# Performance work log

Hardware: AMD Instinct MI355X
Metric: run time of the kernel (lower is better)

## Reference

```python
import jax, jax.numpy as jnp
import numpy as np

N, E, DIM, EDIM = 40000, 640000, 128, 128
EPS = 1e-5

def _layer_norm(x, gamma, beta):
    mu = jnp.mean(x, axis=-1, keepdims=True)
    var = jnp.mean(jnp.square(x - mu), axis=-1, keepdims=True)
    return (x - mu) * jax.lax.rsqrt(var + EPS) * gamma + beta

def setup_inputs() -> dict:
    key = jax.random.key(0)
    ks = jax.random.split(key, 24)
    def lin(k, din, dout):
        k1, k2 = jax.random.split(k)
        lim = 1.0 / np.sqrt(din)
        return (jax.random.uniform(k1, (din, dout), jnp.float32, -lim, lim),
                jax.random.uniform(k2, (dout,), jnp.float32, -lim, lim))
    w_src, b_src = lin(ks[0], DIM, DIM)
    w_dst, b_dst = lin(ks[1], DIM, DIM)
    w_eg,  b_eg  = lin(ks[2], EDIM, DIM)
    w_msg, b_msg = lin(ks[3], DIM, DIM)
    w_n1,  b_n1  = lin(ks[4], 2 * DIM, DIM)
    w_n2,  b_n2  = lin(ks[5], DIM, DIM)
    w_e1,  b_e1  = lin(ks[6], EDIM + 2 * DIM, EDIM)
    w_e2,  b_e2  = lin(ks[7], EDIM, EDIM)
    return {
        'h': jax.random.normal(ks[8], (N, DIM), jnp.float32),
        'e': jax.random.normal(ks[9], (E, EDIM), jnp.float32),
        'src': jax.random.randint(ks[10], (E,), 0, N, jnp.int32),
        'dst': jax.random.randint(ks[11], (E,), 0, N, jnp.int32),
        'w_src': w_src, 'b_src': b_src, 'w_dst': w_dst, 'b_dst': b_dst,
        'w_eg': w_eg, 'b_eg': b_eg, 'w_msg': w_msg, 'b_msg': b_msg,
        'w_n1': w_n1, 'b_n1': b_n1, 'w_n2': w_n2, 'b_n2': b_n2,
        'w_e1': w_e1, 'b_e1': b_e1, 'w_e2': w_e2, 'b_e2': b_e2,
        'g_n': jnp.ones((DIM,), jnp.float32), 'bt_n': jnp.zeros((DIM,), jnp.float32),
        'g_e': jnp.ones((EDIM,), jnp.float32), 'bt_e': jnp.zeros((EDIM,), jnp.float32),
    }

def reference(h, e, src, dst, w_src, b_src, w_dst, b_dst, w_eg, b_eg,
              w_msg, b_msg, w_n1, b_n1, w_n2, b_n2, w_e1, b_e1, w_e2, b_e2,
              g_n, bt_n, g_e, bt_e):
    # Project on nodes once, then gather per edge (same math as projecting gathered feats)
    h_src_proj = h @ w_src + b_src          # [N, DIM]
    h_dst_proj = h @ w_dst + b_dst          # [N, DIM]
    msg_all = h @ w_msg + b_msg             # [N, DIM]
    gate_logits = h_src_proj[src] + h_dst_proj[dst] + (e @ w_eg + b_eg)  # [E, DIM]
    src_msg = msg_all[src]                  # [E, DIM]
    m = jax.nn.sigmoid(gate_logits) * src_msg
    agg = jax.ops.segment_sum(m, dst, num_segments=N)  # [N, DIM]
    nu = jnp.concatenate([h, agg], axis=-1) @ w_n1 + b_n1
    nu = jax.nn.silu(nu) @ w_n2 + b_n2
    h_new = _layer_norm(h + nu, g_n, bt_n)
    e_input = jnp.concatenate([e, src_msg, msg_all[dst]], axis=-1)  # [E, EDIM+2*DIM]
    eu = jax.nn.silu(e_input @ w_e1 + b_e1) @ w_e2 + b_e2
    e_new = _layer_norm(e + eu, g_e, bt_e)
    return h_new, e_new
```

## Files before the change

### kernel.cpp

```cpp
#include <hip/hip_runtime.h>
#include <hip/hip_bf16.h>
#include <stdint.h>

typedef __hip_bfloat16 bf16;
typedef __attribute__((ext_vector_type(8))) short short8;
typedef __attribute__((ext_vector_type(4))) float f32x4;
typedef __attribute__((ext_vector_type(4))) float f4v;

#define DIMN 128
#define BM 64
#define EPSLN 1e-5f

__device__ __forceinline__ float sigm(float x) { return 1.0f / (1.0f + __expf(-x)); }

__device__ __forceinline__ float bfb2f(unsigned short u) {
    union { uint32_t i; float f; } v; v.i = ((uint32_t)u) << 16; return v.f;
}
__device__ __forceinline__ unsigned short f2bfb(float f) {
    union { float f; uint32_t i; } v; v.f = f;
    uint32_t x = v.i;
    return (unsigned short)((x + 0x7FFFu + ((x >> 16) & 1u)) >> 16);
}

template<int F32>
__device__ __forceinline__ float ld(const void* p, size_t i) {
    if (F32) return ((const float*)p)[i];
    else     return bfb2f(((const unsigned short*)p)[i]);
}
template<int F32>
__device__ __forceinline__ void st(void* p, size_t i, float v) {
    if (F32) ((float*)p)[i] = v;
    else     ((unsigned short*)p)[i] = f2bfb(v);
}
template<int F32>
__device__ __forceinline__ void st_nt(void* p, size_t i, float v) {
    if (F32) __builtin_nontemporal_store(v, (float*)p + i);
    else     __builtin_nontemporal_store(f2bfb(v), (unsigned short*)p + i);
}
template<int F32>
__device__ __forceinline__ void load8(const void* p, size_t elem, float v[8]) {
    if (F32) {
        const f4v* q = (const f4v*)((const float*)p + elem);
        f4v a = q[0], b = q[1];
        v[0]=a.x; v[1]=a.y; v[2]=a.z; v[3]=a.w;
        v[4]=b.x; v[5]=b.y; v[6]=b.z; v[7]=b.w;
    } else {
        short8 s = *(const short8*)((const short*)p + elem);
#pragma unroll
        for (int j = 0; j < 8; ++j) v[j] = bfb2f((unsigned short)s[j]);
    }
}
template<int F32>
__device__ __forceinline__ void load8_nt(const void* p, size_t elem, float v[8]) {
    if (F32) {
        const f4v* q = (const f4v*)((const float*)p + elem);
        f4v a = __builtin_nontemporal_load(q);
        f4v b = __builtin_nontemporal_load(q + 1);
        v[0]=a.x; v[1]=a.y; v[2]=a.z; v[3]=a.w;
        v[4]=b.x; v[5]=b.y; v[6]=b.z; v[7]=b.w;
    } else {
        short8 s = __builtin_nontemporal_load((const short8*)((const short*)p + elem));
#pragma unroll
        for (int j = 0; j < 8; ++j) v[j] = bfb2f((unsigned short)s[j]);
    }
}

__device__ __forceinline__ uint32_t xaddr(int r, int k) {
    return (uint32_t)(r * 768 + ((k * 2) ^ ((r & 7) << 4)));
}
__device__ __forceinline__ uint32_t uaddr(int r, int k) {
    return (uint32_t)(r * 768 + 512 + ((k * 2) ^ ((r & 7) << 4)));
}
__device__ __forceinline__ uint32_t haddr(int r, int k) {
    return (uint32_t)(r * 256 + ((k * 2) ^ ((r & 7) << 4)));
}
__device__ __forceinline__ uint32_t x2addr(int r, int k) {
    return (uint32_t)(r * 512 + ((k * 2) ^ ((r & 7) << 4)));
}

__device__ __forceinline__ void atomic_pk_add_bf16(unsigned short* addr, uint32_t data2) {
    unsigned long long a = (unsigned long long)addr;
    asm volatile("global_atomic_pk_add_bf16 %0, %1, off" : : "v"(a), "v"(data2) : "memory");
}

__global__ void detect_dtype_kernel(const uint32_t* __restrict__ w, int* __restrict__ flag) {
    if (threadIdx.x == 0 && blockIdx.x == 0) {
        int c = 0;
        for (int i = 0; i < 64; ++i) {
            uint32_t lo = w[i] & 0xFFFFu;
            int e = (int)((lo >> 7) & 0xFF);
            if (e >= 90 && e <= 140) ++c;
        }
        *flag = (c < 32) ? 1 : 0;
    }
}

template<int F32>
__device__ void prep_body(
    const void* w_eg, const void* w_e1, const void* w_e2,
    const void* w_src, const void* w_dst, const void* w_msg,
    const void* w_n1, const void* w_n2,
    unsigned short* wtg, unsigned short* wt1, unsigned short* wt2,
    unsigned short* wts, unsigned short* wtd, unsigned short* wtm,
    unsigned short* wn1t, unsigned short* wn2t)
{
    int idx = blockIdx.x * 256 + threadIdx.x;
    if (idx < 16384) {
        int c = idx >> 7, k = idx & 127;
        wtg[idx] = f2bfb(ld<F32>(w_eg, (size_t)k * 128 + c));
    } else if (idx < 32768) {
        int i = idx - 16384; int c = i >> 7, k = i & 127;
        wt2[i] = f2bfb(ld<F32>(w_e2, (size_t)k * 128 + c));
    } else if (idx < 81920) {
        int i = idx - 32768; int c = i / 384, k = i % 384;
        wt1[i] = f2bfb(ld<F32>(w_e1, (size_t)k * 128 + c));
    } else if (idx < 98304) {
        int i = idx - 81920; int c = i >> 7, k = i & 127;
        wts[i] = f2bfb(ld<F32>(w_src, (size_t)k * 128 + c));
    } else if (idx < 114688) {
        int i = idx - 98304; int c = i >> 7, k = i & 127;
        wtd[i] = f2bfb(ld<F32>(w_dst, (size_t)k * 128 + c));
    } else if (idx < 131072) {
        int i = idx - 114688; int c = i >> 7, k = i & 127;
        wtm[i] = f2bfb(ld<F32>(w_msg, (size_t)k * 128 + c));
    } else if (idx < 163840) {
        int i = idx - 131072; int c = i >> 8, k = i & 255;
        wn1t[i] = f2bfb(ld<F32>(w_n1, (size_t)k * 128 + c));
    } else if (idx < 180224) {
        int i = idx - 163840; int c = i >> 7, k = i & 127;
        wn2t[i] = f2bfb(ld<F32>(w_n2, (size_t)k * 128 + c));
    }
}
__global__ void __launch_bounds__(256) prep_weights_kernel(
    const int* __restrict__ flag,
    const void* w_eg, const void* w_e1, const void* w_e2,
    const void* w_src, const void* w_dst, const void* w_msg,
    const void* w_n1, const void* w_n2,
    unsigned short* wtg, unsigned short* wt1, unsigned short* wt2,
    unsigned short* wts, unsigned short* wtd, unsigned short* wtm,
    unsigned short* wn1t, unsigned short* wn2t)
{
    if (*flag) prep_body<1>(w_eg, w_e1, w_e2, w_src, w_dst, w_msg, w_n1, w_n2,
                            wtg, wt1, wt2, wts, wtd, wtm, wn1t, wn2t);
    else       prep_body<0>(w_eg, w_e1, w_e2, w_src, w_dst, w_msg, w_n1, w_n2,
                            wtg, wt1, wt2, wts, wtd, wtm, wn1t, wn2t);
}

template<int F32>
__device__ void node_proj_body(
    char* hs,
    const void* h,
    const unsigned short* __restrict__ wts, const unsigned short* __restrict__ wtd,
    const unsigned short* __restrict__ wtm,
    const void* b_src, const void* b_dst, const void* b_msg,
    unsigned short* __restrict__ p_src, unsigned short* __restrict__ p_dst,
    unsigned short* __restrict__ p_msg, int n)
{
    const int tid = threadIdx.x;
    const int base = blockIdx.x * BM;

    for (int idx = tid; idx < BM * 16; idx += 256) {
        int r = idx >> 4, kc = (idx & 15) * 8;
        int row = base + r;
        short8 pk;
        if (row < n) {
            float v[8];
            load8<F32>(h, (size_t)row * 128 + kc, v);
#pragma unroll
            for (int j = 0; j < 8; ++j) pk[j] = (short)f2bfb(v[j]);
        } else {
#pragma unroll
            for (int j = 0; j < 8; ++j) pk[j] = 0;
        }
        *(short8*)(hs + haddr(r, kc)) = pk;
    }
    __syncthreads();

    const int lane = tid & 63;
    const int wv = tid >> 6;
    const int l16 = lane & 15;
    const int lk = lane >> 4;
    const int colbase = wv * 32;

    f32x4 as_[4][2], ad_[4][2], am_[4][2];
#pragma unroll
    for (int mf = 0; mf < 4; ++mf)
#pragma unroll
        for (int nf = 0; nf < 2; ++nf) {
            as_[mf][nf] = (f32x4){0.f,0.f,0.f,0.f};
            ad_[mf][nf] = (f32x4){0.f,0.f,0.f,0.f};
            am_[mf][nf] = (f32x4){0.f,0.f,0.f,0.f};
        }

    for (int kt = 0; kt < 4; ++kt) {
        int k0 = kt * 32;
        short8 a[4];
#pragma unroll
        for (int mf = 0; mf < 4; ++mf)
            a[mf] = *(const short8*)(hs + haddr(mf * 16 + l16, k0 + lk * 8));
        short8 bs0 = *(const short8*)(wts + ((size_t)(colbase + l16)      * 128 + k0 + lk * 8));
        short8 bs1 = *(const short8*)(wts + ((size_t)(colbase + 16 + l16) * 128 + k0 + lk * 8));
        short8 bd0 = *(const short8*)(wtd + ((size_t)(colbase + l16)      * 128 + k0 + lk * 8));
        short8 bd1 = *(const short8*)(wtd + ((size_t)(colbase + 16 + l16) * 128 + k0 + lk * 8));
        short8 bm0 = *(const short8*)(wtm + ((size_t)(colbase + l16)      * 128 + k0 + lk * 8));
        short8 bm1 = *(const short8*)(wtm + ((size_t)(colbase + 16 + l16) * 128 + k0 + lk * 8));
#pragma unroll
        for (int mf = 0; mf < 4; ++mf) {
            as_[mf][0] = __builtin_amdgcn_mfma_f32_16x16x32_bf16(a[mf], bs0, as_[mf][0], 0, 0, 0);
            as_[mf][1] = __builtin_amdgcn_mfma_f32_16x16x32_bf16(a[mf], bs1, as_[mf][1], 0, 0, 0);
            ad_[mf][0] = __builtin_amdgcn_mfma_f32_16x16x32_bf16(a[mf], bd0, ad_[mf][0], 0, 0, 0);
            ad_[mf][1] = __builtin_amdgcn_mfma_f32_16x16x32_bf16(a[mf], bd1, ad_[mf][1], 0, 0, 0);
            am_[mf][0] = __builtin_amdgcn_mfma_f32_16x16x32_bf16(a[mf], bm0, am_[mf][0], 0, 0, 0);
            am_[mf][1] = __builtin_amdgcn_mfma_f32_16x16x32_bf16(a[mf], bm1, am_[mf][1], 0, 0, 0);
        }
    }

    float bsv[2] = { ld<F32>(b_src, colbase + l16), ld<F32>(b_src, colbase + 16 + l16) };
    float bdv[2] = { ld<F32>(b_dst, colbase + l16), ld<F32>(b_dst, colbase + 16 + l16) };
    float bmv[2] = { ld<F32>(b_msg, colbase + l16), ld<F32>(b_msg, colbase + 16 + l16) };
#pragma unroll
    for (int mf = 0; mf < 4; ++mf)
#pragma unroll
        for (int nf = 0; nf < 2; ++nf) {
            int col = colbase + nf * 16 + l16;
#pragma unroll
            for (int rr = 0; rr < 4; ++rr) {
                int row = mf * 16 + lk * 4 + rr;
                if (base + row < n) {
                    size_t o = (size_t)(base + row) * 128 + col;
                    p_src[o] = f2bfb(as_[mf][nf][rr] + bsv[nf]);
                    p_dst[o] = f2bfb(ad_[mf][nf][rr] + bdv[nf]);
                    p_msg[o] = f2bfb(am_[mf][nf][rr] + bmv[nf]);
                }
            }
        }
}
__global__ void __launch_bounds__(256, 4) node_proj_kernel(
    const int* __restrict__ flag,
    const void* h,
    const unsigned short* wts, const unsigned short* wtd, const unsigned short* wtm,
    const void* b_src, const void* b_dst, const void* b_msg,
    unsigned short* p_src, unsigned short* p_dst, unsigned short* p_msg, int n)
{
    __shared__ short hs_raw[BM * 128];
    char* hs = (char*)hs_raw;
    if (*flag) node_proj_body<1>(hs, h, wts, wtd, wtm, b_src, b_dst, b_msg, p_src, p_dst, p_msg, n);
    else       node_proj_body<0>(hs, h, wts, wtd, wtm, b_src, b_dst, b_msg, p_src, p_dst, p_msg, n);
}

template<int F32>
__device__ void edge_mega_body(
    char* xs, int* sidx, int* didx,
    float* sm_s, float* sm_s2, float* sm_mu, float* sm_rs, float* bge_s,
    const void* e,
    const int* __restrict__ src, const int* __restrict__ dst,
    const unsigned short* __restrict__ p_src, const unsigned short* __restrict__ p_dst,
    const unsigned short* __restrict__ p_msg,
    const unsigned short* __restrict__ wtg,
    const unsigned short* __restrict__ wt1,
    const unsigned short* __restrict__ wt2,
    const void* b_eg, const void* b_e1, const void* b_e2,
    const void* g_e, const void* bt_e,
    unsigned short* __restrict__ agg, void* out, size_t obase, int ne)
{
    const int tid = threadIdx.x;
    const int base = blockIdx.x * BM;

    if (tid < BM) {
        int eid = base + tid;
        sidx[tid] = (eid < ne) ? src[eid] : 0;
        didx[tid] = (eid < ne) ? dst[eid] : 0;
        sm_s[tid] = 0.f; sm_s2[tid] = 0.f;
    }
    if (tid >= 128 && tid < 256) bge_s[tid - 128] = ld<F32>(b_eg, tid - 128);
    __syncthreads();

    const int gr = tid >> 2, gq = tid & 3;
    const int gc0 = gq * 32;
    short8 psv[4], pdv[4];
    {
        const unsigned short* ps = p_src + (size_t)sidx[gr] * 128 + gc0;
        const unsigned short* pd = p_dst + (size_t)didx[gr] * 128 + gc0;
#pragma unroll
        for (int i = 0; i < 4; ++i) {
            psv[i] = *(const short8*)(ps + 8 * i);
            pdv[i] = *(const short8*)(pd + 8 * i);
        }
    }

    for (int idx = tid; idx < BM * 48; idx += 256) {
        int r = idx / 48;
        int kc = (idx % 48) * 8;
        int eid = base + r;
        short8 pk;
        if (eid < ne) {
            if (kc < 128) {
                float v[8];
                load8_nt<F32>(e, (size_t)eid * 128 + kc, v);
#pragma unroll
                for (int j = 0; j < 8; ++j) pk[j] = (short)f2bfb(v[j]);
            } else if (kc < 256) {
                pk = *(const short8*)(p_msg + (size_t)sidx[r] * 128 + (kc - 128));
            } else {
                pk = *(const short8*)(p_msg + (size_t)didx[r] * 128 + (kc - 256));
            }
        } else {
#pragma unroll
            for (int j = 0; j < 8; ++j) pk[j] = 0;
        }
        *(short8*)(xs + xaddr(r, kc)) = pk;
    }
    __syncthreads();

    const int lane = tid & 63;
    const int wv = tid >> 6;
    const int l16 = lane & 15;
    const int lk = lane >> 4;
    const int colbase = wv * 32;

    f32x4 acc1[4][2], accg[4][2];
#pragma unroll
    for (int mf = 0; mf < 4; ++mf)
#pragma unroll
        for (int nf = 0; nf < 2; ++nf) {
            acc1[mf][nf] = (f32x4){0.f,0.f,0.f,0.f};
            accg[mf][nf] = (f32x4){0.f,0.f,0.f,0.f};
        }

    for (int kt = 0; kt < 12; ++kt) {
        int k0 = kt * 32;
        short8 a[4];
#pragma unroll
        for (int mf = 0; mf < 4; ++mf)
            a[mf] = *(const short8*)(xs + xaddr(mf * 16 + l16, k0 + lk * 8));
        short8 b0 = *(const short8*)(wt1 + ((size_t)(colbase + l16)      * 384 + k0 + lk * 8));
        short8 b1 = *(const short8*)(wt1 + ((size_t)(colbase + 16 + l16) * 384 + k0 + lk * 8));
#pragma unroll
        for (int mf = 0; mf < 4; ++mf) {
            acc1[mf][0] = __builtin_amdgcn_mfma_f32_16x16x32_bf16(a[mf], b0, acc1[mf][0], 0, 0, 0);
            acc1[mf][1] = __builtin_amdgcn_mfma_f32_16x16x32_bf16(a[mf], b1, acc1[mf][1], 0, 0, 0);
        }
        if (kt < 4) {
            short8 g0 = *(const short8*)(wtg + ((size_t)(colbase + l16)      * 128 + k0 + lk * 8));
            short8 g1 = *(const short8*)(wtg + ((size_t)(colbase + 16 + l16) * 128 + k0 + lk * 8));
#pragma unroll
            for (int mf = 0; mf < 4; ++mf) {
                accg[mf][0] = __builtin_amdgcn_mfma_f32_16x16x32_bf16(a[mf], g0, accg[mf][0], 0, 0, 0);
                accg[mf][1] = __builtin_amdgcn_mfma_f32_16x16x32_bf16(a[mf], g1, accg[mf][1], 0, 0, 0);
            }
        }
    }
    __syncthreads();

#pragma unroll
    for (int mf = 0; mf < 4; ++mf)
#pragma unroll
        for (int nf = 0; nf < 2; ++nf) {
            int col = colbase + nf * 16 + l16;
#pragma unroll
            for (int rr = 0; rr < 4; ++rr) {
                int row = mf * 16 + lk * 4 + rr;
                *(unsigned short*)(xs + uaddr(row, col)) = f2bfb(accg[mf][nf][rr]);
            }
        }
    __syncthreads();

    {
        int eid = base + gr;
        if (eid < ne) {
            short8 pmv[4], agv[4];
#pragma unroll
            for (int i = 0; i < 4; ++i) {
                pmv[i] = *(const short8*)(xs + xaddr(gr, 128 + gc0 + 8 * i));
                agv[i] = *(const short8*)(xs + uaddr(gr, gc0 + 8 * i));
            }
#pragma unroll
            for (int i = 0; i < 4; ++i) {
                short8 mv;
#pragma unroll
                for (int j = 0; j < 8; ++j) {
                    int c = gc0 + 8 * i + j;
                    float g = bfb2f((unsigned short)agv[i][j]) + bge_s[c]
                            + bfb2f((unsigned short)psv[i][j])
                            + bfb2f((unsigned short)pdv[i][j]);
                    float m = sigm(g) * bfb2f((unsigned short)pmv[i][j]);
                    mv[j] = (short)f2bfb(m);
                }
                *(short8*)(xs + xaddr(gr, 128 + gc0 + 8 * i)) = mv;
            }
        }
    }
    __syncthreads();

    {
        float be1[2] = { ld<F32>(b_e1, colbase + l16), ld<F32>(b_e1, colbase + 16 + l16) };
#pragma unroll
        for (int mf = 0; mf < 4; ++mf)
#pragma unroll
            for (int nf = 0; nf < 2; ++nf) {
                int col = colbase + nf * 16 + l16;
#pragma unroll
                for (int rr = 0; rr < 4; ++rr) {
                    int row = mf * 16 + lk * 4 + rr;
                    float u = acc1[mf][nf][rr] + be1[nf];
                    u = u * sigm(u);
                    *(unsigned short*)(xs + uaddr(row, col)) = f2bfb(u);
                }
            }
    }
    __syncthreads();

    f32x4 acc2[4][2];
#pragma unroll
    for (int mf = 0; mf < 4; ++mf)
#pragma unroll
        for (int nf = 0; nf < 2; ++nf) acc2[mf][nf] = (f32x4){0.f,0.f,0.f,0.f};

    for (int kt = 0; kt < 4; ++kt) {
        int k0 = kt * 32;
        short8 a[4];
#pragma unroll
        for (int mf = 0; mf < 4; ++mf)
            a[mf] = *(const short8*)(xs + uaddr(mf * 16 + l16, k0 + lk * 8));
        short8 b0 = *(const short8*)(wt2 + ((size_t)(colbase + l16)      * 128 + k0 + lk * 8));
        short8 b1 = *(const short8*)(wt2 + ((size_t)(colbase + 16 + l16) * 128 + k0 + lk * 8));
#pragma unroll
        for (int mf = 0; mf < 4; ++mf) {
            acc2[mf][0] = __builtin_amdgcn_mfma_f32_16x16x32_bf16(a[mf], b0, acc2[mf][0], 0, 0, 0);
            acc2[mf][1] = __builtin_amdgcn_mfma_f32_16x16x32_bf16(a[mf], b1, acc2[mf][1], 0, 0, 0);
        }
    }

    float xv[4][2][4];
    {
        float be2[2] = { ld<F32>(b_e2, colbase + l16), ld<F32>(b_e2, colbase + 16 + l16) };
#pragma unroll
        for (int mf = 0; mf < 4; ++mf)
#pragma unroll
            for (int nf = 0; nf < 2; ++nf) {
                int col = colbase + nf * 16 + l16;
#pragma unroll
                for (int rr = 0; rr < 4; ++rr) {
                    int row = mf * 16 + lk * 4 + rr;
                    unsigned short eb = *(const unsigned short*)(xs + xaddr(row, col));
                    xv[mf][nf][rr] = bfb2f(eb) + acc2[mf][nf][rr] + be2[nf];
                }
            }
    }
#pragma unroll
    for (int mf = 0; mf < 4; ++mf)
#pragma unroll
        for (int rr = 0; rr < 4; ++rr) {
            float v0 = xv[mf][0][rr], v1 = xv[mf][1][rr];
            float s = v0 + v1;
            float s2 = v0 * v0 + v1 * v1;
#pragma unroll
            for (int off = 1; off < 16; off <<= 1) {
                s  += __shfl_xor(s, off, 16);
                s2 += __shfl_xor(s2, off, 16);
            }
            if (l16 == 0) {
                int row = mf * 16 + lk * 4 + rr;
                atomicAdd(&sm_s[row], s);
                atomicAdd(&sm_s2[row], s2);
            }
        }
    __syncthreads();
    if (tid < BM) {
        float mu = sm_s[tid] * (1.f / 128.f);
        float var = sm_s2[tid] * (1.f / 128.f) - mu * mu;
        sm_mu[tid] = mu;
        sm_rs[tid] = rsqrtf(var + EPSLN);
    }
    __syncthreads();

    {
        float ge[2]  = { ld<F32>(g_e, colbase + l16),  ld<F32>(g_e, colbase + 16 + l16) };
        float bte[2] = { ld<F32>(bt_e, colbase + l16), ld<F32>(bt_e, colbase + 16 + l16) };
#pragma unroll
        for (int mf = 0; mf < 4; ++mf)
#pragma unroll
            for (int nf = 0; nf < 2; ++nf) {
                int col = colbase + nf * 16 + l16;
#pragma unroll
                for (int rr = 0; rr < 4; ++rr) {
                    int row = mf * 16 + lk * 4 + rr;
                    int eid = base + row;
                    float o = (xv[mf][nf][rr] - sm_mu[row]) * sm_rs[row] * ge[nf] + bte[nf];
                    if (eid < ne) st_nt<F32>(out, obase + (size_t)eid * 128 + col, o);
                }
            }
    }

    {
        int col2 = (tid & 63) * 2;
        int r0 = (tid >> 6) * 16;
        for (int rr = 0; rr < 16; ++rr) {
            int row = r0 + rr;
            int eid = base + row;
            if (eid < ne) {
                uint32_t m2 = *(const uint32_t*)(xs + xaddr(row, 128 + col2));
                atomic_pk_add_bf16(agg + (size_t)didx[row] * 128 + col2, m2);
            }
        }
    }
}
__global__ void __launch_bounds__(256, 3) edge_mega_kernel(
    const int* __restrict__ flag,
    const void* e, const int* src, const int* dst,
    const unsigned short* p_src, const unsigned short* p_dst, const unsigned short* p_msg,
    const unsigned short* wtg, const unsigned short* wt1, const unsigned short* wt2,
    const void* b_eg, const void* b_e1, const void* b_e2,
    const void* g_e, const void* bt_e,
    unsigned short* agg, void* out, size_t obase, int ne)
{
    __shared__ short xs_raw[BM * 384];
    __shared__ int sidx[BM], didx[BM];
    __shared__ float sm_s[BM], sm_s2[BM], sm_mu[BM], sm_rs[BM];
    __shared__ float bge_s[128];
    char* xs = (char*)xs_raw;
    if (*flag) edge_mega_body<1>(xs, sidx, didx, sm_s, sm_s2, sm_mu, sm_rs, bge_s,
                                 e, src, dst, p_src, p_dst, p_msg, wtg, wt1, wt2,
                                 b_eg, b_e1, b_e2, g_e, bt_e, agg, out, obase, ne);
    else       edge_mega_body<0>(xs, sidx, didx, sm_s, sm_s2, sm_mu, sm_rs, bge_s,
                                 e, src, dst, p_src, p_dst, p_msg, wtg, wt1, wt2,
                                 b_eg, b_e1, b_e2, g_e, bt_e, agg, out, obase, ne);
}

template<int F32>
__device__ void node_update_body(
    char* xs, float* sm_s, float* sm_s2, float* sm_mu, float* sm_rs,
    const void* h, const unsigned short* __restrict__ agg,
    const unsigned short* __restrict__ wn1t, const unsigned short* __restrict__ wn2t,
    const void* b_n1, const void* b_n2,
    const void* g_n, const void* bt_n, void* out, int n)
{
    const int tid = threadIdx.x;
    const int base = blockIdx.x * BM;

    if (tid < BM) { sm_s[tid] = 0.f; sm_s2[tid] = 0.f; }

    for (int idx = tid; idx < BM * 32; idx += 256) {
        int r = idx >> 5, kc = (idx & 31) * 8;
        int row = base + r;
        short8 pk;
        if (row < n) {
            if (kc < 128) {
                float v[8];
                load8<F32>(h, (size_t)row * 128 + kc, v);
#pragma unroll
                for (int j = 0; j < 8; ++j) pk[j] = (short)f2bfb(v[j]);
            } else {
                pk = *(const short8*)(agg + (size_t)row * 128 + (kc - 128));
            }
        } else {
#pragma unroll
            for (int j = 0; j < 8; ++j) pk[j] = 0;
        }
        *(short8*)(xs + x2addr(r, kc)) = pk;
    }
    __syncthreads();

    const int lane = tid & 63;
    const int wv = tid >> 6;
    const int l16 = lane & 15;
    const int lk = lane >> 4;
    const int colbase = wv * 32;

    f32x4 acc1[4][2];
#pragma unroll
    for (int mf = 0; mf < 4; ++mf)
#pragma unroll
        for (int nf = 0; nf < 2; ++nf) acc1[mf][nf] = (f32x4){0.f,0.f,0.f,0.f};

    for (int kt = 0; kt < 8; ++kt) {
        int k0 = kt * 32;
        short8 a[4];
#pragma unroll
        for (int mf = 0; mf < 4; ++mf)
            a[mf] = *(const short8*)(xs + x2addr(mf * 16 + l16, k0 + lk * 8));
        short8 b0 = *(const short8*)(wn1t + ((size_t)(colbase + l16)      * 256 + k0 + lk * 8));
        short8 b1 = *(const short8*)(wn1t + ((size_t)(colbase + 16 + l16) * 256 + k0 + lk * 8));
#pragma unroll
        for (int mf = 0; mf < 4; ++mf) {
            acc1[mf][0] = __builtin_amdgcn_mfma_f32_16x16x32_bf16(a[mf], b0, acc1[mf][0], 0, 0, 0);
            acc1[mf][1] = __builtin_amdgcn_mfma_f32_16x16x32_bf16(a[mf], b1, acc1[mf][1], 0, 0, 0);
        }
    }
    __syncthreads();

    {
        float b1v[2] = { ld<F32>(b_n1, colbase + l16), ld<F32>(b_n1, colbase + 16 + l16) };
#pragma unroll
        for (int mf = 0; mf < 4; ++mf)
#pragma unroll
            for (int nf = 0; nf < 2; ++nf) {
                int col = colbase + nf * 16 + l16;
#pragma unroll
                for (int rr = 0; rr < 4; ++rr) {
                    int row = mf * 16 + lk * 4 + rr;
                    float u = acc1[mf][nf][rr] + b1v[nf];
                    u = u * sigm(u);
                    *(unsigned short*)(xs + x2addr(row, 128 + col)) = f2bfb(u);
                }
            }
    }
    __syncthreads();

    f32x4 acc2[4][2];
#pragma unroll
    for (int mf = 0; mf < 4; ++mf)
#pragma unroll
        for (int nf = 0; nf < 2; ++nf) acc2[mf][nf] = (f32x4){0.f,0.f,0.f,0.f};

    for (int kt = 0; kt < 4; ++kt) {
        int k0 = kt * 32;
        short8 a[4];
#pragma unroll
        for (int mf = 0; mf < 4; ++mf)
            a[mf] = *(const short8*)(xs + x2addr(mf * 16 + l16, 128 + k0 + lk * 8));
        short8 b0 = *(const short8*)(wn2t + ((size_t)(colbase + l16)      * 128 + k0 + lk * 8));
        short8 b1 = *(const short8*)(wn2t + ((size_t)(colbase + 16 + l16) * 128 + k0 + lk * 8));
#pragma unroll
        for (int mf = 0; mf < 4; ++mf) {
            acc2[mf][0] = __builtin_amdgcn_mfma_f32_16x16x32_bf16(a[mf], b0, acc2[mf][0], 0, 0, 0);
            acc2[mf][1] = __builtin_amdgcn_mfma_f32_16x16x32_bf16(a[mf], b1, acc2[mf][1], 0, 0, 0);
        }
    }

    float xv[4][2][4];
    {
        float b2v[2] = { ld<F32>(b_n2, colbase + l16), ld<F32>(b_n2, colbase + 16 + l16) };
#pragma unroll
        for (int mf = 0; mf < 4; ++mf)
#pragma unroll
            for (int nf = 0; nf < 2; ++nf) {
                int col = colbase + nf * 16 + l16;
#pragma unroll
                for (int rr = 0; rr < 4; ++rr) {
                    int row = mf * 16 + lk * 4 + rr;
                    unsigned short hb = *(const unsigned short*)(xs + x2addr(row, col));
                    xv[mf][nf][rr] = bfb2f(hb) + acc2[mf][nf][rr] + b2v[nf];
                }
            }
    }
#pragma unroll
    for (int mf = 0; mf < 4; ++mf)
#pragma unroll
        for (int rr = 0; rr < 4; ++rr) {
            float v0 = xv[mf][0][rr], v1 = xv[mf][1][rr];
            float s = v0 + v1;
            float s2 = v0 * v0 + v1 * v1;
#pragma unroll
            for (int off = 1; off < 16; off <<= 1) {
                s  += __shfl_xor(s, off, 16);
                s2 += __shfl_xor(s2, off, 16);
            }
            if (l16 == 0) {
                int row = mf * 16 + lk * 4 + rr;
                atomicAdd(&sm_s[row], s);
                atomicAdd(&sm_s2[row], s2);
            }
        }
    __syncthreads();
    if (tid < BM) {
        float mu = sm_s[tid] * (1.f / 128.f);
        float var = sm_s2[tid] * (1.f / 128.f) - mu * mu;
        sm_mu[tid] = mu;
        sm_rs[tid] = rsqrtf(var + EPSLN);
    }
    __syncthreads();
    {
        float gn[2]  = { ld<F32>(g_n, colbase + l16),  ld<F32>(g_n, colbase + 16 + l16) };
        float btn[2] = { ld<F32>(bt_n, colbase + l16), ld<F32>(bt_n, colbase + 16 + l16) };
#pragma unroll
        for (int mf = 0; mf < 4; ++mf)
#pragma unroll
            for (int nf = 0; nf < 2; ++nf) {
                int col = colbase + nf * 16 + l16;
#pragma unroll
                for (int rr = 0; rr < 4; ++rr) {
                    int row = mf * 16 + lk * 4 + rr;
                    float o = (xv[mf][nf][rr] - sm_mu[row]) * sm_rs[row] * gn[nf] + btn[nf];
                    if (base + row < n)
                        st_nt<F32>(out, (size_t)(base + row) * 128 + col, o);
                }
            }
    }
}
__global__ void __launch_bounds__(256, 4) node_update_kernel(
    const int* __restrict__ flag,
    const void* h, const unsigned short* agg,
    const unsigned short* wn1t, const unsigned short* wn2t,
    const void* b_n1, const void* b_n2,
    const void* g_n, const void* bt_n, void* out, int n)
{
    __shared__ short x2_raw[BM * 256];
    __shared__ float sm_s[BM], sm_s2[BM], sm_mu[BM], sm_rs[BM];
    char* xs = (char*)x2_raw;
    if (*flag) node_update_body<1>(xs, sm_s, sm_s2, sm_mu, sm_rs, h, agg, wn1t, wn2t,
                                   b_n1, b_n2, g_n, bt_n, out, n);
    else       node_update_body<0>(xs, sm_s, sm_s2, sm_mu, sm_rs, h, agg, wn1t, wn2t,
                                   b_n1, b_n2, g_n, bt_n, out, n);
}

extern "C" void kernel_launch(void* const* d_in, const int* in_sizes, int n_in,
                              void* d_out, int out_size, void* d_ws, size_t ws_size,
                              hipStream_t stream)
{
    const void* h     = d_in[0];
    const void* e     = d_in[1];
    const int*  src   = (const int*)d_in[2];
    const int*  dst   = (const int*)d_in[3];
    const void* w_src = d_in[4];
    const void* b_src = d_in[5];
    const void* w_dst = d_in[6];
    const void* b_dst = d_in[7];
    const void* w_eg  = d_in[8];
    const void* b_eg  = d_in[9];
    const void* w_msg = d_in[10];
    const void* b_msg = d_in[11];
    const void* w_n1  = d_in[12];
    const void* b_n1  = d_in[13];
    const void* w_n2  = d_in[14];
    const void* b_n2  = d_in[15];
    const void* w_e1  = d_in[16];
    const void* b_e1  = d_in[17];
    const void* w_e2  = d_in[18];
    const void* b_e2  = d_in[19];
    const void* g_n   = d_in[20];
    const void* bt_n  = d_in[21];
    const void* g_e   = d_in[22];
    const void* bt_e  = d_in[23];

    const int n  = in_sizes[0] / DIMN;
    const int ne = in_sizes[1] / DIMN;

    char* ws = (char*)d_ws;
    unsigned short* p_src = (unsigned short*)ws;       ws += (size_t)n * DIMN * 2;
    unsigned short* p_dst = (unsigned short*)ws;       ws += (size_t)n * DIMN * 2;
    unsigned short* p_msg = (unsigned short*)ws;       ws += (size_t)n * DIMN * 2;
    unsigned short* agg   = (unsigned short*)ws;       ws += (size_t)n * DIMN * 2;
    int*   flag  = (int*)ws;                           ws += 256;
    unsigned short* wtg  = (unsigned short*)ws;        ws += 128 * 128 * 2;
    unsigned short* wt2  = (unsigned short*)ws;        ws += 128 * 128 * 2;
    unsigned short* wt1  = (unsigned short*)ws;        ws += 128 * 384 * 2;
    unsigned short* wts  = (unsigned short*)ws;        ws += 128 * 128 * 2;
    unsigned short* wtd  = (unsigned short*)ws;        ws += 128 * 128 * 2;
    unsigned short* wtm  = (unsigned short*)ws;        ws += 128 * 128 * 2;
    unsigned short* wn1t = (unsigned short*)ws;        ws += 128 * 256 * 2;
    unsigned short* wn2t = (unsigned short*)ws;        ws += 128 * 128 * 2;

    hipMemsetAsync(agg, 0, (size_t)n * DIMN * sizeof(unsigned short), stream);

    detect_dtype_kernel<<<1, 64, 0, stream>>>((const uint32_t*)h, flag);

    prep_weights_kernel<<<704, 256, 0, stream>>>(
        flag, w_eg, w_e1, w_e2, w_src, w_dst, w_msg, w_n1, w_n2,
        wtg, wt1, wt2, wts, wtd, wtm, wn1t, wn2t);

    int nb_n = (n + BM - 1) / BM;
    int nb_e = (ne + BM - 1) / BM;

    node_proj_kernel<<<nb_n, 256, 0, stream>>>(
        flag, h, wts, wtd, wtm, b_src, b_dst, b_msg, p_src, p_dst, p_msg, n);

    edge_mega_kernel<<<nb_e, 256, 0, stream>>>(
        flag, e, src, dst, p_src, p_dst, p_msg, wtg, wt1, wt2,
        b_eg, b_e1, b_e2, g_e, bt_e, agg, d_out, (size_t)n * DIMN, ne);

    node_update_kernel<<<nb_n, 256, 0, stream>>>(
        flag, h, agg, wn1t, wn2t, b_n1, b_n2, g_n, bt_n, d_out, n);
}
```

Measured before the change: 700.9 us.

## Precompute per-node msg projections through edge MLP weights to shrink edge GEMM K

Pushes the src_msg and msg_all[dst] slices of the first edge MLP layer from per-edge to per-node work. The node projection kernel now computes q_b = p_msg·W1[128:256] and q_c = p_msg·W1[256:384], and the edge kernel gathers these instead of running a K=384 GEMM, reducing edge MFMA work from 12 to 4 k-steps. Edge shared memory drops from 48KB to 32KB, the agg atomics move earlier, and launch bounds rise to 4 blocks per SM. In exchange there are two more bf16 gathers per edge, extra node-side GEMMs, and an added bf16 rounding of q_b/q_c before the sum.

Measured after the change: 785.5 us. 12.1% more time.

```diff
diff --git a/kernel.cpp b/kernel.cpp
--- a/kernel.cpp
+++ b/kernel.cpp
@@ -26,11 +26,6 @@
 __device__ __forceinline__ float ld(const void* p, size_t i) {
     if (F32) return ((const float*)p)[i];
     else     return bfb2f(((const unsigned short*)p)[i]);
-}
-template<int F32>
-__device__ __forceinline__ void st(void* p, size_t i, float v) {
-    if (F32) ((float*)p)[i] = v;
-    else     ((unsigned short*)p)[i] = f2bfb(v);
 }
 template<int F32>
 __device__ __forceinline__ void st_nt(void* p, size_t i, float v) {
@@ -65,13 +60,7 @@
     }
 }
 
-__device__ __forceinline__ uint32_t xaddr(int r, int k) {
-    return (uint32_t)(r * 768 + ((k * 2) ^ ((r & 7) << 4)));
-}
-__device__ __forceinline__ uint32_t uaddr(int r, int k) {
-    return (uint32_t)(r * 768 + 512 + ((k * 2) ^ ((r & 7) << 4)));
-}
-__device__ __forceinline__ uint32_t haddr(int r, int k) {
+__device__ __forceinline__ uint32_t taddr(int r, int k) {
     return (uint32_t)(r * 256 + ((k * 2) ^ ((r & 7) << 4)));
 }
 __device__ __forceinline__ uint32_t x2addr(int r, int k) {
@@ -151,10 +140,11 @@
     char* hs,
     const void* h,
     const unsigned short* __restrict__ wts, const unsigned short* __restrict__ wtd,
-    const unsigned short* __restrict__ wtm,
+    const unsigned short* __restrict__ wtm, const unsigned short* __restrict__ wt1,
     const void* b_src, const void* b_dst, const void* b_msg,
     unsigned short* __restrict__ p_src, unsigned short* __restrict__ p_dst,
-    unsigned short* __restrict__ p_msg, int n)
+    unsigned short* __restrict__ p_msg,
+    unsigned short* __restrict__ q_b, unsigned short* __restrict__ q_c, int n)
 {
     const int tid = threadIdx.x;
     const int base = blockIdx.x * BM;
@@ -172,7 +162,7 @@
 #pragma unroll
             for (int j = 0; j < 8; ++j) pk[j] = 0;
         }
-        *(short8*)(hs + haddr(r, kc)) = pk;
+        *(short8*)(hs + taddr(r, kc)) = pk;
     }
     __syncthreads();
 
@@ -197,7 +187,7 @@
         short8 a[4];
 #pragma unroll
         for (int mf = 0; mf < 4; ++mf)
-            a[mf] = *(const short8*)(hs + haddr(mf * 16 + l16, k0 + lk * 8));
+            a[mf] = *(const short8*)(hs + taddr(mf * 16 + l16, k0 + lk * 8));
         short8 bs0 = *(const short8*)(wts + ((size_t)(colbase + l16)      * 128 + k0 + lk * 8));
         short8 bs1 = *(const short8*)(wts + ((size_t)(colbase + 16 + l16) * 128 + k0 + lk * 8));
         short8 bd0 = *(const short8*)(wtd + ((size_t)(colbase + l16)      * 128 + k0 + lk * 8));
@@ -218,6 +208,66 @@
     float bsv[2] = { ld<F32>(b_src, colbase + l16), ld<F32>(b_src, colbase + 16 + l16) };
     float bdv[2] = { ld<F32>(b_dst, colbase + l16), ld<F32>(b_dst, colbase + 16 + l16) };
     float bmv[2] = { ld<F32>(b_msg, colbase + l16), ld<F32>(b_msg, colbase + 16 + l16) };
+    float pm[4][2][4];
+#pragma unroll
+    for (int mf = 0; mf < 4; ++mf)
+#pragma unroll
+        for (int nf = 0; nf < 2; ++nf) {
+            int col = colbase + nf * 16 + l16;
+#pragma unroll
+            for (int rr = 0; rr < 4; ++rr) {
+                int row = mf * 16 + lk * 4 + rr;
+                float pmv_ = am_[mf][nf][rr] + bmv[nf];
+                pm[mf][nf][rr] = pmv_;
+                if (base + row < n) {
+                    size_t o = (size_t)(base + row) * 128 + col;
+                    p_src[o] = f2bfb(as_[mf][nf][rr] + bsv[nf]);
+                    p_dst[o] = f2bfb(ad_[mf][nf][rr] + bdv[nf]);
+                    p_msg[o] = f2bfb(pmv_);
+                }
+            }
+        }
+    __syncthreads();
+
+#pragma unroll
+    for (int mf = 0; mf < 4; ++mf)
+#pragma unroll
+        for (int nf = 0; nf < 2; ++nf) {
+            int col = colbase + nf * 16 + l16;
+#pragma unroll
+            for (int rr = 0; rr < 4; ++rr) {
+                int row = mf * 16 + lk * 4 + rr;
+                *(unsigned short*)(hs + taddr(row, col)) = f2bfb(pm[mf][nf][rr]);
+            }
+        }
+    __syncthreads();
+
+    f32x4 qb_[4][2], qc_[4][2];
+#pragma unroll
+    for (int mf = 0; mf < 4; ++mf)
+#pragma unroll
+        for (int nf = 0; nf < 2; ++nf) {
+            qb_[mf][nf] = (f32x4){0.f,0.f,0.f,0.f};
+            qc_[mf][nf] = (f32x4){0.f,0.f,0.f,0.f};
+        }
+    for (int kt = 0; kt < 4; ++kt) {
+        int k0 = kt * 32;
+        short8 a[4];
+#pragma unroll
+        for (int mf = 0; mf < 4; ++mf)
+            a[mf] = *(const short8*)(hs + taddr(mf * 16 + l16, k0 + lk * 8));
+        short8 qb0 = *(const short8*)(wt1 + ((size_t)(colbase + l16)      * 384 + 128 + k0 + lk * 8));
+        short8 qb1 = *(const short8*)(wt1 + ((size_t)(colbase + 16 + l16) * 384 + 128 + k0 + lk * 8));
+        short8 qc0 = *(const short8*)(wt1 + ((size_t)(colbase + l16)      * 384 + 256 + k0 + lk * 8));
+        short8 qc1 = *(const short8*)(wt1 + ((size_t)(colbase + 16 + l16) * 384 + 256 + k0 + lk * 8));
+#pragma unroll
+        for (int mf = 0; mf < 4; ++mf) {
+            qb_[mf][0] = __builtin_amdgcn_mfma_f32_16x16x32_bf16(a[mf], qb0, qb_[mf][0], 0, 0, 0);
+            qb_[mf][1] = __builtin_amdgcn_mfma_f32_16x16x32_bf16(a[mf], qb1, qb_[mf][1], 0, 0, 0);
+            qc_[mf][0] = __builtin_amdgcn_mfma_f32_16x16x32_bf16(a[mf], qc0, qc_[mf][0], 0, 0, 0);
+            qc_[mf][1] = __builtin_amdgcn_mfma_f32_16x16x32_bf16(a[mf], qc1, qc_[mf][1], 0, 0, 0);
+        }
+    }
 #pragma unroll
     for (int mf = 0; mf < 4; ++mf)
 #pragma unroll
@@ -228,9 +278,8 @@
                 int row = mf * 16 + lk * 4 + rr;
                 if (base + row < n) {
                     size_t o = (size_t)(base + row) * 128 + col;
-                    p_src[o] = f2bfb(as_[mf][nf][rr] + bsv[nf]);
-                    p_dst[o] = f2bfb(ad_[mf][nf][rr] + bdv[nf]);
-                    p_msg[o] = f2bfb(am_[mf][nf][rr] + bmv[nf]);
+                    q_b[o] = f2bfb(qb_[mf][nf][rr]);
+                    q_c[o] = f2bfb(qc_[mf][nf][rr]);
                 }
             }
         }
@@ -239,28 +288,33 @@
     const int* __restrict__ flag,
     const void* h,
     const unsigned short* wts, const unsigned short* wtd, const unsigned short* wtm,
+    const unsigned short* wt1,
     const void* b_src, const void* b_dst, const void* b_msg,
-    unsigned short* p_src, unsigned short* p_dst, unsigned short* p_msg, int n)
+    unsigned short* p_src, unsigned short* p_dst, unsigned short* p_msg,
+    unsigned short* q_b, unsigned short* q_c, int n)
 {
     __shared__ short hs_raw[BM * 128];
     char* hs = (char*)hs_raw;
-    if (*flag) node_proj_body<1>(hs, h, wts, wtd, wtm, b_src, b_dst, b_msg, p_src, p_dst, p_msg, n);
-    else       node_proj_body<0>(hs, h, wts, wtd, wtm, b_src, b_dst, b_msg, p_src, p_dst, p_msg, n);
+    if (*flag) node_proj_body<1>(hs, h, wts, wtd, wtm, wt1, b_src, b_dst, b_msg,
+                                 p_src, p_dst, p_msg, q_b, q_c, n);
+    else       node_proj_body<0>(hs, h, wts, wtd, wtm, wt1, b_src, b_dst, b_msg,
+                                 p_src, p_dst, p_msg, q_b, q_c, n);
 }
 
 template<int F32>
 __device__ void edge_mega_body(
-    char* xs, int* sidx, int* didx,
-    float* sm_s, float* sm_s2, float* sm_mu, float* sm_rs, float* bge_s,
+    char* es, char* r2, int* sidx, int* didx,
+    float* sm_s, float* sm_s2, float* sm_mu, float* sm_rs,
+    float* bge_s, float* be1_s,
     const void* e,
     const int* __restrict__ src, const int* __restrict__ dst,
     const unsigned short* __restrict__ p_src, const unsigned short* __restrict__ p_dst,
     const unsigned short* __restrict__ p_msg,
+    const unsigned short* __restrict__ q_b, const unsigned short* __restrict__ q_c,
     const unsigned short* __restrict__ wtg,
     const unsigned short* __restrict__ wt1,
     const unsigned short* __restrict__ wt2,
-    const void* b_eg, const void* b_e1, const void* b_e2,
-    const void* g_e, const void* bt_e,
+    const void* b_e2, const void* g_e, const void* bt_e,
     unsigned short* __restrict__ agg, void* out, size_t obase, int ne)
 {
     const int tid = threadIdx.x;
@@ -272,43 +326,37 @@
         didx[tid] = (eid < ne) ? dst[eid] : 0;
         sm_s[tid] = 0.f; sm_s2[tid] = 0.f;
     }
-    if (tid >= 128 && tid < 256) bge_s[tid - 128] = ld<F32>(b_eg, tid - 128);
     __syncthreads();
 
     const int gr = tid >> 2, gq = tid & 3;
     const int gc0 = gq * 32;
-    short8 psv[4], pdv[4];
+    short8 psv[4], pdv[4], pmv[4];
     {
         const unsigned short* ps = p_src + (size_t)sidx[gr] * 128 + gc0;
         const unsigned short* pd = p_dst + (size_t)didx[gr] * 128 + gc0;
+        const unsigned short* pmp = p_msg + (size_t)sidx[gr] * 128 + gc0;
 #pragma unroll
         for (int i = 0; i < 4; ++i) {
             psv[i] = *(const short8*)(ps + 8 * i);
             pdv[i] = *(const short8*)(pd + 8 * i);
-        }
-    }
-
-    for (int idx = tid; idx < BM * 48; idx += 256) {
-        int r = idx / 48;
-        int kc = (idx % 48) * 8;
+            pmv[i] = *(const short8*)(pmp + 8 * i);
+        }
+    }
+
+    for (int idx = tid; idx < BM * 16; idx += 256) {
+        int r = idx >> 4, kc = (idx & 15) * 8;
         int eid = base + r;
         short8 pk;
         if (eid < ne) {
-            if (kc < 128) {
-                float v[8];
-                load8_nt<F32>(e, (size_t)eid * 128 + kc, v);
-#pragma unroll
-                for (int j = 0; j < 8; ++j) pk[j] = (short)f2bfb(v[j]);
-            } else if (kc < 256) {
-                pk = *(const short8*)(p_msg + (size_t)sidx[r] * 128 + (kc - 128));
-            } else {
-                pk = *(const short8*)(p_msg + (size_t)didx[r] * 128 + (kc - 256));
-            }
+            float v[8];
+            load8_nt<F32>(e, (size_t)eid * 128 + kc, v);
+#pragma unroll
+            for (int j = 0; j < 8; ++j) pk[j] = (short)f2bfb(v[j]);
         } else {
 #pragma unroll
             for (int j = 0; j < 8; ++j) pk[j] = 0;
         }
-        *(short8*)(xs + xaddr(r, kc)) = pk;
+        *(short8*)(es + taddr(r, kc)) = pk;
     }
     __syncthreads();
 
@@ -327,30 +375,24 @@
             accg[mf][nf] = (f32x4){0.f,0.f,0.f,0.f};
         }
 
-    for (int kt = 0; kt < 12; ++kt) {
+    for (int kt = 0; kt < 4; ++kt) {
         int k0 = kt * 32;
         short8 a[4];
 #pragma unroll
         for (int mf = 0; mf < 4; ++mf)
-            a[mf] = *(const short8*)(xs + xaddr(mf * 16 + l16, k0 + lk * 8));
+            a[mf] = *(const short8*)(es + taddr(mf * 16 + l16, k0 + lk * 8));
         short8 b0 = *(const short8*)(wt1 + ((size_t)(colbase + l16)      * 384 + k0 + lk * 8));
         short8 b1 = *(const short8*)(wt1 + ((size_t)(colbase + 16 + l16) * 384 + k0 + lk * 8));
+        short8 g0 = *(const short8*)(wtg + ((size_t)(colbase + l16)      * 128 + k0 + lk * 8));
+        short8 g1 = *(const short8*)(wtg + ((size_t)(colbase + 16 + l16) * 128 + k0 + lk * 8));
 #pragma unroll
         for (int mf = 0; mf < 4; ++mf) {
             acc1[mf][0] = __builtin_amdgcn_mfma_f32_16x16x32_bf16(a[mf], b0, acc1[mf][0], 0, 0, 0);
             acc1[mf][1] = __builtin_amdgcn_mfma_f32_16x16x32_bf16(a[mf], b1, acc1[mf][1], 0, 0, 0);
-        }
-        if (kt < 4) {
-            short8 g0 = *(const short8*)(wtg + ((size_t)(colbase + l16)      * 128 + k0 + lk * 8));
-            short8 g1 = *(const short8*)(wtg + ((size_t)(colbase + 16 + l16) * 128 + k0 + lk * 8));
-#pragma unroll
-            for (int mf = 0; mf < 4; ++mf) {
-                accg[mf][0] = __builtin_amdgcn_mfma_f32_16x16x32_bf16(a[mf], g0, accg[mf][0], 0, 0, 0);
-                accg[mf][1] = __builtin_amdgcn_mfma_f32_16x16x32_bf16(a[mf], g1, accg[mf][1], 0, 0, 0);
-            }
-        }
-    }
-    __syncthreads();
+            accg[mf][0] = __builtin_amdgcn_mfma_f32_16x16x32_bf16(a[mf], g0, accg[mf][0], 0, 0, 0);
+            accg[mf][1] = __builtin_amdgcn_mfma_f32_16x16x32_bf16(a[mf], g1, accg[mf][1], 0, 0, 0);
+        }
+    }
 
 #pragma unroll
     for (int mf = 0; mf < 4; ++mf)
@@ -360,7 +402,7 @@
 #pragma unroll
             for (int rr = 0; rr < 4; ++rr) {
                 int row = mf * 16 + lk * 4 + rr;
-                *(unsigned short*)(xs + uaddr(row, col)) = f2bfb(accg[mf][nf][rr]);
+                *(unsigned short*)(r2 + taddr(row, col)) = f2bfb(accg[mf][nf][rr]);
             }
         }
     __syncthreads();
@@ -368,12 +410,10 @@
     {
         int eid = base + gr;
         if (eid < ne) {
-            short8 pmv[4], agv[4];
-#pragma unroll
-            for (int i = 0; i < 4; ++i) {
-                pmv[i] = *(const short8*)(xs + xaddr(gr, 128 + gc0 + 8 * i));
-                agv[i] = *(const short8*)(xs + uaddr(gr, gc0 + 8 * i));
-            }
+            short8 agv[4];
+#pragma unroll
+            for (int i = 0; i < 4; ++i)
+                agv[i] = *(const short8*)(r2 + taddr(gr, gc0 + 8 * i));
 #pragma unroll
             for (int i = 0; i < 4; ++i) {
                 short8 mv;
@@ -386,27 +426,72 @@
                     float m = sigm(g) * bfb2f((unsigned short)pmv[i][j]);
                     mv[j] = (short)f2bfb(m);
                 }
-                *(short8*)(xs + xaddr(gr, 128 + gc0 + 8 * i)) = mv;
-            }
-        }
-    }
-    __syncthreads();
-
-    {
-        float be1[2] = { ld<F32>(b_e1, colbase + l16), ld<F32>(b_e1, colbase + 16 + l16) };
-#pragma unroll
-        for (int mf = 0; mf < 4; ++mf)
-#pragma unroll
-            for (int nf = 0; nf < 2; ++nf) {
-                int col = colbase + nf * 16 + l16;
-#pragma unroll
-                for (int rr = 0; rr < 4; ++rr) {
-                    int row = mf * 16 + lk * 4 + rr;
-                    float u = acc1[mf][nf][rr] + be1[nf];
+                *(short8*)(r2 + taddr(gr, gc0 + 8 * i)) = mv;
+            }
+        }
+    }
+    short8 qbv[4], qcv[4];
+    {
+        const unsigned short* qb = q_b + (size_t)sidx[gr] * 128 + gc0;
+        const unsigned short* qc = q_c + (size_t)didx[gr] * 128 + gc0;
+#pragma unroll
+        for (int i = 0; i < 4; ++i) {
+            qbv[i] = *(const short8*)(qb + 8 * i);
+            qcv[i] = *(const short8*)(qc + 8 * i);
+        }
+    }
+    __syncthreads();
+
+    {
+        int col2 = (tid & 63) * 2;
+        int r0 = (tid >> 6) * 16;
+        for (int rr = 0; rr < 16; ++rr) {
+            int row = r0 + rr;
+            int eid = base + row;
+            if (eid < ne) {
+                uint32_t m2 = *(const uint32_t*)(r2 + taddr(row, col2));
+                atomic_pk_add_bf16(agg + (size_t)didx[row] * 128 + col2, m2);
+            }
+        }
+    }
+    __syncthreads();
+
+#pragma unroll
+    for (int mf = 0; mf < 4; ++mf)
+#pragma unroll
+        for (int nf = 0; nf < 2; ++nf) {
+            int col = colbase + nf * 16 + l16;
+#pragma unroll
+            for (int rr = 0; rr < 4; ++rr) {
+                int row = mf * 16 + lk * 4 + rr;
+                *(unsigned short*)(r2 + taddr(row, col)) = f2bfb(acc1[mf][nf][rr]);
+            }
+        }
+    __syncthreads();
+
+    {
+        int eid = base + gr;
+        if (eid < ne) {
+            short8 a1v[4];
+#pragma unroll
+            for (int i = 0; i < 4; ++i)
+                a1v[i] = *(const short8*)(r2 + taddr(gr, gc0 + 8 * i));
+#pragma unroll
+            for (int i = 0; i < 4; ++i) {
+                short8 uv;
+#pragma unroll
+                for (int j = 0; j < 8; ++j) {
+                    int c = gc0 + 8 * i + j;
+                    float u = bfb2f((unsigned short)a1v[i][j])
+                            + bfb2f((unsigned short)qbv[i][j])
+                            + bfb2f((unsigned short)qcv[i][j])
+                            + be1_s[c];
                     u = u * sigm(u);
-                    *(unsigned short*)(xs + uaddr(row, col)) = f2bfb(u);
+                    uv[j] = (short)f2bfb(u);
                 }
-            }
+                *(short8*)(r2 + taddr(gr, gc0 + 8 * i)) = uv;
+            }
+        }
     }
     __syncthreads();
 
@@ -421,7 +506,7 @@
         short8 a[4];
 #pragma unroll
         for (int mf = 0; mf < 4; ++mf)
-            a[mf] = *(const short8*)(xs + uaddr(mf * 16 + l16, k0 + lk * 8));
+            a[mf] = *(const short8*)(r2 + taddr(mf * 16 + l16, k0 + lk * 8));
         short8 b0 = *(const short8*)(wt2 + ((size_t)(colbase + l16)      * 128 + k0 + lk * 8));
         short8 b1 = *(const short8*)(wt2 + ((size_t)(colbase + 16 + l16) * 128 + k0 + lk * 8));
 #pragma unroll
@@ -442,7 +527,7 @@
 #pragma unroll
                 for (int rr = 0; rr < 4; ++rr) {
                     int row = mf * 16 + lk * 4 + rr;
-                    unsigned short eb = *(const unsigned short*)(xs + xaddr(row, col));
+                    unsigned short eb = *(const unsigned short*)(es + taddr(row, col));
                     xv[mf][nf][rr] = bfb2f(eb) + acc2[mf][nf][rr] + be2[nf];
                 }
             }
@@ -491,40 +576,54 @@
                 }
             }
     }
-
-    {
-        int col2 = (tid & 63) * 2;
-        int r0 = (tid >> 6) * 16;
-        for (int rr = 0; rr < 16; ++rr) {
-            int row = r0 + rr;
-            int eid = base + row;
-            if (eid < ne) {
-                uint32_t m2 = *(const uint32_t*)(xs + xaddr(row, 128 + col2));
-                atomic_pk_add_bf16(agg + (size_t)didx[row] * 128 + col2, m2);
-            }
-        }
-    }
-}
-__global__ void __launch_bounds__(256, 3) edge_mega_kernel(
-    const int* __restrict__ flag,
+}
+
+template<int F32>
+__device__ void edge_mega_entry(
+    char* es, char* r2, int* sidx, int* didx,
+    float* sm_s, float* sm_s2, float* sm_mu, float* sm_rs,
+    float* bge_s, float* be1_s,
     const void* e, const int* src, const int* dst,
     const unsigned short* p_src, const unsigned short* p_dst, const unsigned short* p_msg,
+    const unsigned short* q_b, const unsigned short* q_c,
     const unsigned short* wtg, const unsigned short* wt1, const unsigned short* wt2,
     const void* b_eg, const void* b_e1, const void* b_e2,
     const void* g_e, const void* bt_e,
     unsigned short* agg, void* out, size_t obase, int ne)
 {
-    __shared__ short xs_raw[BM * 384];
+    int tid = threadIdx.x;
+    if (tid >= 128 && tid < 256) {
+        bge_s[tid - 128] = ld<F32>(b_eg, tid - 128);
+        be1_s[tid - 128] = ld<F32>(b_e1, tid - 128);
+    }
+    edge_mega_body<F32>(es, r2, sidx, didx, sm_s, sm_s2, sm_mu, sm_rs, bge_s, be1_s,
+                        e, src, dst, p_src, p_dst, p_msg, q_b, q_c, wtg, wt1, wt2,
+                        b_e2, g_e, bt_e, agg, out, obase, ne);
+}
+
+__global__ void __launch_bounds__(256, 4) edge_mega_kernel(
+    const int* __restrict__ flag,
+    const void* e, const int* src, const int* dst,
+    const unsigned short* p_src, const unsigned short* p_dst, const unsigned short* p_msg,
+    const unsigned short* q_b, const unsigned short* q_c,
+    const unsigned short* wtg, const unsigned short* wt1, const unsigned short* wt2,
+    const void* b_eg, const void* b_e1, const void* b_e2,
+    const void* g_e, const void* bt_e,
+    unsigned short* agg, void* out, size_t obase, int ne)
+{
+    __shared__ short es_raw[BM * 128];
+    __shared__ short r2_raw[BM * 128];
     __shared__ int sidx[BM], didx[BM];
     __shared__ float sm_s[BM], sm_s2[BM], sm_mu[BM], sm_rs[BM];
-    __shared__ float bge_s[128];
-    char* xs = (char*)xs_raw;
-    if (*flag) edge_mega_body<1>(xs, sidx, didx, sm_s, sm_s2, sm_mu, sm_rs, bge_s,
-                                 e, src, dst, p_src, p_dst, p_msg, wtg, wt1, wt2,
-                                 b_eg, b_e1, b_e2, g_e, bt_e, agg, out, obase, ne);
-    else       edge_mega_body<0>(xs, sidx, didx, sm_s, sm_s2, sm_mu, sm_rs, bge_s,
-                                 e, src, dst, p_src, p_dst, p_msg, wtg, wt1, wt2,
-                                 b_eg, b_e1, b_e2, g_e, bt_e, agg, out, obase, ne);
+    __shared__ float bge_s[128], be1_s[128];
+    char* es = (char*)es_raw;
+    char* r2 = (char*)r2_raw;
+    if (*flag) edge_mega_entry<1>(es, r2, sidx, didx, sm_s, sm_s2, sm_mu, sm_rs, bge_s, be1_s,
+                                  e, src, dst, p_src, p_dst, p_msg, q_b, q_c, wtg, wt1, wt2,
+                                  b_eg, b_e1, b_e2, g_e, bt_e, agg, out, obase, ne);
+    else       edge_mega_entry<0>(es, r2, sidx, didx, sm_s, sm_s2, sm_mu, sm_rs, bge_s, be1_s,
+                                  e, src, dst, p_src, p_dst, p_msg, q_b, q_c, wtg, wt1, wt2,
+                                  b_eg, b_e1, b_e2, g_e, bt_e, agg, out, obase, ne);
 }
 
 template<int F32>
@@ -740,6 +839,8 @@
     unsigned short* p_src = (unsigned short*)ws;       ws += (size_t)n * DIMN * 2;
     unsigned short* p_dst = (unsigned short*)ws;       ws += (size_t)n * DIMN * 2;
     unsigned short* p_msg = (unsigned short*)ws;       ws += (size_t)n * DIMN * 2;
+    unsigned short* q_b   = (unsigned short*)ws;       ws += (size_t)n * DIMN * 2;
+    unsigned short* q_c   = (unsigned short*)ws;       ws += (size_t)n * DIMN * 2;
     unsigned short* agg   = (unsigned short*)ws;       ws += (size_t)n * DIMN * 2;
     int*   flag  = (int*)ws;                           ws += 256;
     unsigned short* wtg  = (unsigned short*)ws;        ws += 128 * 128 * 2;
@@ -763,10 +864,11 @@
     int nb_e = (ne + BM - 1) / BM;
 
     node_proj_kernel<<<nb_n, 256, 0, stream>>>(
-        flag, h, wts, wtd, wtm, b_src, b_dst, b_msg, p_src, p_dst, p_msg, n);
+        flag, h, wts, wtd, wtm, wt1, b_src, b_dst, b_msg,
+        p_src, p_dst, p_msg, q_b, q_c, n);
 
     edge_mega_kernel<<<nb_e, 256, 0, stream>>>(
-        flag, e, src, dst, p_src, p_dst, p_msg, wtg, wt1, wt2,
+        flag, e, src, dst, p_src, p_dst, p_msg, q_b, q_c, wtg, wt1, wt2,
         b_eg, b_e1, b_e2, g_e, bt_e, agg, d_out, (size_t)n * DIMN, ne);
 
     node_update_kernel<<<nb_n, 256, 0, stream>>>(
```
